# Kernel optimization log

Hardware: AMD Instinct MI355X
Metric: run time of the kernel (lower is better)

Reference implementation:

```python
import jax, jax.numpy as jnp
import numpy as np

B_, L_, DM = 8, 1024, 256
DS, DC, EX = 16, 4, 2
DI = EX * DM            # d_inner = 512
DTR = max(1, DM // 16)  # dt_rank = 16


def setup_inputs() -> dict:
    key = jax.random.key(0)
    ks = iter(jax.random.split(key, 40))
    def n(shape, s=0.02):
        return jax.random.normal(next(ks), shape, jnp.float32) * s
    inp = {"x": jax.random.normal(next(ks), (B_, L_, DM), jnp.float32)}
    inp["norm_g"] = jnp.ones((DM,), jnp.float32)
    inp["norm_b"] = jnp.zeros((DM,), jnp.float32)
    for m in ("f", "b"):
        inp[f"inW_{m}"] = n((DM, 2 * DI))
        inp[f"convW_{m}"] = n((DI, DC))
        inp[f"convB_{m}"] = jnp.zeros((DI,), jnp.float32)
        inp[f"xW_{m}"] = n((DI, DTR + 2 * DS))
        inp[f"dtW_{m}"] = n((DTR, DI))
        inp[f"dtB_{m}"] = jnp.zeros((DI,), jnp.float32)
        # ALog init: log of [1..dState] repeated over dInner rows
        inp[f"ALog_{m}"] = jnp.log(jnp.tile(jnp.arange(1, DS + 1, dtype=jnp.float32), (DI, 1)))
        inp[f"Dp_{m}"] = jnp.ones((DI,), jnp.float32)
        inp[f"outW_{m}"] = n((DI, DM))
    inp["fusW"] = n((2 * DM, DM))
    inp["fusB"] = jnp.zeros((DM,), jnp.float32)
    return inp


def _dw_conv(x, w, b):
    # causal depthwise conv1d: x [B,L,DI], w [DI,DC] -> [B,L,DI]
    xc = jnp.transpose(x, (0, 2, 1))  # B,DI,L
    out = jax.lax.conv_general_dilated(
        xc, w[:, None, :], window_strides=(1,), padding=[(DC - 1, 0)],
        dimension_numbers=("NCH", "OIH", "NCH"), feature_group_count=DI)
    return jnp.transpose(out + b[:, None], (0, 2, 1))


def _ssm(x, xW, dtW, dtB, ALog, Dp):
    # x: [B,L,DI]
    A = -jnp.exp(ALog)                                   # [DI,DS]
    xdbl = x @ xW                                        # [B,L,DTR+2*DS]
    dlt, Bp, Cp = jnp.split(xdbl, [DTR, DTR + DS], axis=-1)
    delta = jax.nn.softplus(dlt @ dtW + dtB)             # [B,L,DI]
    dA = jnp.exp(delta[..., None] * A)                   # [B,L,DI,DS]
    dBx = (delta * x)[..., None] * Bp[:, :, None, :]     # [B,L,DI,DS]

    def step(h, t):
        a, bb, c = t
        h = a * h + bb                                   # [B,DI,DS]
        y = jnp.einsum('bdn,bn->bd', h, c)
        return h, y

    h0 = jnp.zeros((x.shape[0], DI, DS), x.dtype)
    _, ys = jax.lax.scan(step, h0, (jnp.moveaxis(dA, 1, 0),
                                    jnp.moveaxis(dBx, 1, 0),
                                    jnp.moveaxis(Cp, 1, 0)))
    return jnp.moveaxis(ys, 0, 1) + Dp * x               # [B,L,DI]


def _mamba(x, inW, convW, convB, xW, dtW, dtB, ALog, Dp, outW):
    xr = x @ inW                                         # [B,L,2*DI]
    xs, res = jnp.split(xr, 2, axis=-1)
    xs = jax.nn.silu(_dw_conv(xs, convW, convB))
    y = _ssm(xs, xW, dtW, dtB, ALog, Dp)
    return (y * jax.nn.silu(res)) @ outW                 # [B,L,DM]


def reference(x, norm_g, norm_b,
              inW_f, convW_f, convB_f, xW_f, dtW_f, dtB_f, ALog_f, Dp_f, outW_f,
              inW_b, convW_b, convB_b, xW_b, dtW_b, dtB_b, ALog_b, Dp_b, outW_b,
              fusW, fusB):
    # LayerNorm
    mu = x.mean(-1, keepdims=True)
    var = ((x - mu) ** 2).mean(-1, keepdims=True)
    xn = (x - mu) * jax.lax.rsqrt(var + 1e-5) * norm_g + norm_b
    # forward-direction Mamba
    xf = _mamba(xn, inW_f, convW_f, convB_f, xW_f, dtW_f, dtB_f, ALog_f, Dp_f, outW_f)
    # backward-direction Mamba (flip along time)
    xb = _mamba(jnp.flip(xn, 1), inW_b, convW_b, convB_b, xW_b, dtW_b, dtB_b, ALog_b, Dp_b, outW_b)
    xb = jnp.flip(xb, 1)
    fused = jnp.concatenate([xf, xb], axis=-1) @ fusW + fusB
    return x + fused  # dropout is identity in eval
```

## Files before the change

### kernel.cpp

```cpp
#include <hip/hip_runtime.h>
#include <cmath>

typedef __bf16 bf16x8 __attribute__((ext_vector_type(8)));
typedef __bf16 bf16x4 __attribute__((ext_vector_type(4)));
typedef float  f32x4  __attribute__((ext_vector_type(4)));
typedef float  f32x2  __attribute__((ext_vector_type(2)));

#define B_  8
#define L_  1024
#define DM  256
#define DI  512
#define DS  16
#define DTR 16
#define M_  (B_*L_)
#define NC  32
#define CT  32

__device__ inline float softplus_f(float z){
  return (z > 20.f) ? z : __logf(1.f + __expf(z));
}
__device__ inline float silu_f(float z){
  return z / (1.f + __expf(-z));
}

__device__ inline int flag_from_x(const void* x){
  const unsigned short* u = (const unsigned short*)x;
  int lane = threadIdx.x & 63;
  unsigned short v = u[2*lane];
  int e = (v >> 7) & 0xFF;
  unsigned long long m = __ballot(e >= 160 || e < 96);
  return __popcll(m) > 16;
}

struct PrepJob { const void* src; void* dst; int rows; int cols; int f32out; };
struct PrepArgs { PrepJob j[26]; int nj; };
struct TJob { const void* src; __bf16* dst; int R; int C; };
struct TArgs { TJob j[3]; int ntiles[3]; int nj; int ntot; };

__global__ __launch_bounds__(256) void wprep_k(TArgs ta, PrepArgs a, const void* xsrc){
  const int f = flag_from_x(xsrc);
  const int tid = threadIdx.x;
  if ((int)blockIdx.x < ta.ntot){
    __shared__ float tile[64][65];
    int bid = blockIdx.x;
    int jj = 0;
    while (jj < ta.nj-1 && bid >= ta.ntiles[jj]) { bid -= ta.ntiles[jj]; jj++; }
    const TJob J = ta.j[jj];
    const int tpr = J.C >> 6;
    const int tr = bid / tpr, tc = bid - tr*tpr;
    const int r0 = tr*64, c0 = tc*64;
    #pragma unroll
    for (int i=0;i<16;i++){
      int idx = i*256 + tid;
      int r = idx >> 6, c = idx & 63;
      long off = (long)(r0+r)*J.C + c0 + c;
      tile[r][c] = f ? ((const float*)J.src)[off] : (float)((const __bf16*)J.src)[off];
    }
    __syncthreads();
    #pragma unroll
    for (int i=0;i<16;i++){
      int idx = i*256 + tid;
      int c = idx >> 6, r = idx & 63;
      J.dst[(long)(c0+c)*J.R + r0 + r] = (__bf16)tile[r][c];
    }
  } else {
    int e = (blockIdx.x - ta.ntot)*256 + tid;
    #pragma unroll 1
    for (int jj=0; jj<a.nj; jj++){
      int sz = a.j[jj].rows * a.j[jj].cols;
      if (e < sz){
        int cols = a.j[jj].cols;
        int r = e / cols, c = e - r*cols;
        float v = f ? ((const float*)a.j[jj].src)[e] : (float)((const __bf16*)a.j[jj].src)[e];
        if (a.j[jj].f32out) ((float*)a.j[jj].dst)[c*a.j[jj].rows + r] = v;
        else ((__bf16*)a.j[jj].dst)[(long)c*a.j[jj].rows + r] = (__bf16)v;
        return;
      }
      e -= sz;
    }
  }
}

__global__ __launch_bounds__(256) void lnw_k(
    const void* x, const __bf16* g, const __bf16* bb, __bf16* xn,
    const __bf16* fusWt, const __bf16* outWr0, const __bf16* outWr1,
    __bf16* BtC0, __bf16* BtC1)
{
  const int bx = blockIdx.x;
  const int tid = threadIdx.x;
  const int lane = tid & 63;
  const int wid = tid >> 6;

  if (bx < M_/4){
    const int f = flag_from_x(x);
    long row = (long)bx*4 + wid;
    long base = row*DM + lane*4;
    float v0,v1,v2,v3;
    if (f){ f32x4 xv = *(const f32x4*)((const float*)x + base);
            v0=xv[0]; v1=xv[1]; v2=xv[2]; v3=xv[3]; }
    else  { bf16x4 xv = *(const bf16x4*)((const __bf16*)x + base);
            v0=(float)xv[0]; v1=(float)xv[1]; v2=(float)xv[2]; v3=(float)xv[3]; }
    float s = v0+v1+v2+v3;
    float q = v0*v0+v1*v1+v2*v2+v3*v3;
    #pragma unroll
    for (int off=32; off>0; off>>=1){ s += __shfl_xor(s,off); q += __shfl_xor(q,off); }
    float mu = s*(1.f/DM), var = q*(1.f/DM)-mu*mu;
    float rs = rsqrtf(var+1e-5f);
    bf16x4 gv = *(const bf16x4*)(g + lane*4);
    bf16x4 bv = *(const bf16x4*)(bb + lane*4);
    bf16x4 o;
    o[0]=(__bf16)((v0-mu)*rs*(float)gv[0]+(float)bv[0]);
    o[1]=(__bf16)((v1-mu)*rs*(float)gv[1]+(float)bv[1]);
    o[2]=(__bf16)((v2-mu)*rs*(float)gv[2]+(float)bv[2]);
    o[3]=(__bf16)((v3-mu)*rs*(float)gv[3]+(float)bv[3]);
    *(bf16x4*)(xn + base) = o;
  } else {
    int b2 = bx - M_/4;
    int wz  = b2 >> 5;
    int rem = b2 & 31;
    int gx = rem & 3, gy = rem >> 2;
    const __bf16* A  = fusWt + wz*DM;
    const __bf16* Bt = wz ? outWr1 : outWr0;
    __bf16* C = wz ? BtC1 : BtC0;
    const int mBase = (gx*4 + wid)*16;
    const int nBase = gy*64;
    const int lm = lane & 15;
    const int kq = (lane >> 4)*8;
    long aoff = (long)(mBase+lm)*(2*DM) + kq;
    long boff[4];
    #pragma unroll
    for (int j=0;j<4;j++) boff[j] = (long)(nBase+j*16+lm)*DM + kq;
    f32x4 acc[4] = {};
    #pragma unroll
    for (int k0=0;k0<DM;k0+=32){
      bf16x8 af = *(const bf16x8*)(A + aoff + k0);
      bf16x8 bfr[4];
      #pragma unroll
      for (int j=0;j<4;j++) bfr[j] = *(const bf16x8*)(Bt + boff[j] + k0);
      #pragma unroll
      for (int j=0;j<4;j++)
        acc[j] = __builtin_amdgcn_mfma_f32_16x16x32_bf16(af, bfr[j], acc[j], 0,0,0);
    }
    #pragma unroll
    for (int rr=0;rr<4;rr++){
      int r = mBase + (lane>>4)*4 + rr;
      #pragma unroll
      for (int j=0;j<4;j++){
        int c = nBase + j*16 + lm;
        C[(long)r*DI + c] = (__bf16)acc[j][rr];
      }
    }
  }
}

template<int BM,int BN,int KK>
__global__ __launch_bounds__(256) void gemm_in_k(
    const __bf16* A, const __bf16* B0, const __bf16* B1,
    __bf16* xz0, __bf16* xz1, __bf16* res0, __bf16* res1,
    int lda, int ldb)
{
  constexpr int TM = BM/2, TN = BN/2;
  constexpr int WMT = TM/16, WNT = TN/16;
  constexpr int LA = BM/64, LB = BN/64;

  const int dir = blockIdx.z;
  const __bf16* Bt = dir ? B1 : B0;
  __bf16* xz  = dir ? xz1 : xz0;
  __bf16* res = dir ? res1 : res0;
  const int tid  = threadIdx.x;
  const int lane = tid & 63;
  const int wid  = tid >> 6;
  const int wm = wid & 1;
  const int wn = wid >> 1;
  const int mBase = blockIdx.x * BM;
  const int nBase = blockIdx.y * BN;
  const int lm = lane & 15;
  const int kq = (lane >> 4) * 8;

  __shared__ __bf16 As[BM*32];
  __shared__ __bf16 Bs[BN*32];

  const __bf16* aS[LA];
  const __bf16* bS[LB];
  {
    int colk = (tid & 3) * 8;
    #pragma unroll
    for (int ld=0; ld<LA; ld++){
      int r = mBase + ld*64 + (tid >> 2);
      if (dir==1){ int b = r >> 10, t = r & (L_-1); r = (b<<10) + (L_-1-t); }
      aS[ld] = A + (long)r*lda + colk;
    }
    #pragma unroll
    for (int ld=0; ld<LB; ld++){
      int r = nBase + ld*64 + (tid >> 2);
      bS[ld] = Bt + (long)r*ldb + colk;
    }
  }

  f32x4 acc[WMT][WNT] = {};
  for (int k0=0; k0<KK; k0+=32){
    #pragma unroll
    for (int ld=0; ld<LA; ld++)
      __builtin_amdgcn_global_load_lds(
        (const __attribute__((address_space(1))) void*)(aS[ld] + k0),
        (__attribute__((address_space(3))) void*)(&As[ld*2048 + tid*8]), 16, 0, 0);
    #pragma unroll
    for (int ld=0; ld<LB; ld++)
      __builtin_amdgcn_global_load_lds(
        (const __attribute__((address_space(1))) void*)(bS[ld] + k0),
        (__attribute__((address_space(3))) void*)(&Bs[ld*2048 + tid*8]), 16, 0, 0);
    __syncthreads();
    bf16x8 af[WMT], bfr[WNT];
    #pragma unroll
    for (int i=0;i<WMT;i++) af[i]  = *(const bf16x8*)&As[(wm*TM + i*16 + lm)*32 + kq];
    #pragma unroll
    for (int j=0;j<WNT;j++) bfr[j] = *(const bf16x8*)&Bs[(wn*TN + j*16 + lm)*32 + kq];
    #pragma unroll
    for (int i=0;i<WMT;i++)
      #pragma unroll
      for (int j=0;j<WNT;j++)
        acc[i][j] = __builtin_amdgcn_mfma_f32_16x16x32_bf16(af[i], bfr[j], acc[i][j], 0,0,0);
    __syncthreads();
  }

  #pragma unroll
  for (int i=0;i<WMT;i++){
    #pragma unroll
    for (int rr=0;rr<4;rr++){
      int r = mBase + wm*TM + i*16 + (lane>>4)*4 + rr;
      #pragma unroll
      for (int j=0;j<WNT;j++){
        int c = nBase + wn*TN + j*16 + lm;
        float v = acc[i][j][rr];
        if (c < DI) xz[(long)r*DI + c] = (__bf16)v;
        else        res[(long)r*DI + (c-DI)] = (__bf16)v;
      }
    }
  }
}

template<int BM,int BN,int KK>
__global__ __launch_bounds__(256) void gemm_fin_k(
    const __bf16* Af, const __bf16* Ab,
    const __bf16* Bt0, const __bf16* Bt1,
    void* Cout, const __bf16* bias, const void* resid)
{
  constexpr int TM = BM/2, TN = BN/2;
  constexpr int WMT = TM/16, WNT = TN/16;
  constexpr int LA = BM/64, LB = BN/64;

  const int of = flag_from_x(resid);
  const int tid  = threadIdx.x;
  const int lane = tid & 63;
  const int wid  = tid >> 6;
  const int wm = wid & 1;
  const int wn = wid >> 1;
  const int mBase = blockIdx.x * BM;
  const int nBase = blockIdx.y * BN;
  const int lm = lane & 15;
  const int kq = (lane >> 4) * 8;

  __shared__ __bf16 As[BM*32];
  __shared__ __bf16 Bs[BN*32];

  f32x4 acc[WMT][WNT] = {};
  #pragma unroll 1
  for (int dd=0; dd<2; dd++){
    const __bf16* A  = dd ? Ab  : Af;
    const __bf16* Bt = dd ? Bt1 : Bt0;
    const __bf16* aS[LA];
    const __bf16* bS[LB];
    {
      int colk = (tid & 3) * 8;
      #pragma unroll
      for (int ld=0; ld<LA; ld++){
        int r = mBase + ld*64 + (tid >> 2);
        if (dd==1){ int b = r >> 10, t = r & (L_-1); r = (b<<10) + (L_-1-t); }
        aS[ld] = A + (long)r*DI + colk;
      }
      #pragma unroll
      for (int ld=0; ld<LB; ld++){
        int r = nBase + ld*64 + (tid >> 2);
        bS[ld] = Bt + (long)r*DI + colk;
      }
    }
    for (int k0=0; k0<KK; k0+=32){
      #pragma unroll
      for (int ld=0; ld<LA; ld++)
        __builtin_amdgcn_global_load_lds(
          (const __attribute__((address_space(1))) void*)(aS[ld] + k0),
          (__attribute__((address_space(3))) void*)(&As[ld*2048 + tid*8]), 16, 0, 0);
      #pragma unroll
      for (int ld=0; ld<LB; ld++)
        __builtin_amdgcn_global_load_lds(
          (const __attribute__((address_space(1))) void*)(bS[ld] + k0),
          (__attribute__((address_space(3))) void*)(&Bs[ld*2048 + tid*8]), 16, 0, 0);
      __syncthreads();
      bf16x8 af[WMT], bfr[WNT];
      #pragma unroll
      for (int i=0;i<WMT;i++) af[i]  = *(const bf16x8*)&As[(wm*TM + i*16 + lm)*32 + kq];
      #pragma unroll
      for (int j=0;j<WNT;j++) bfr[j] = *(const bf16x8*)&Bs[(wn*TN + j*16 + lm)*32 + kq];
      #pragma unroll
      for (int i=0;i<WMT;i++)
        #pragma unroll
        for (int j=0;j<WNT;j++)
          acc[i][j] = __builtin_amdgcn_mfma_f32_16x16x32_bf16(af[i], bfr[j], acc[i][j], 0,0,0);
      __syncthreads();
    }
  }

  #pragma unroll
  for (int i=0;i<WMT;i++){
    #pragma unroll
    for (int rr=0;rr<4;rr++){
      int r = mBase + wm*TM + i*16 + (lane>>4)*4 + rr;
      #pragma unroll
      for (int j=0;j<WNT;j++){
        int c = nBase + wn*TN + j*16 + lm;
        float v = acc[i][j][rr];
        float rsd = of ? ((const float*)resid)[(long)r*DM + c]
                       : (float)((const __bf16*)resid)[(long)r*DM + c];
        v += (float)bias[c] + rsd;
        if (of) ((float*)Cout)[(long)r*DM + c] = v;
        else    ((__bf16*)Cout)[(long)r*DM + c] = (__bf16)v;
      }
    }
  }
}

__global__ __launch_bounds__(512) void scanA_k(
    const __bf16* xz0, const __bf16* xz1,
    const float* cw0, const float* cw1,
    const __bf16* cb0, const __bf16* cb1,
    const __bf16* xW0, const __bf16* xW1,
    const float* dw0, const float* dw1,
    const __bf16* dtB0, const __bf16* dtB1,
    const float* ALf0, const float* ALf1,
    __bf16* xg0, __bf16* xg1,
    float* sg0, float* sg1,
    float* hend, float* sumd)
{
  const int dir = blockIdx.z;
  const __bf16* xz  = dir ? xz1 : xz0;
  const float*  cw  = dir ? cw1 : cw0;
  const __bf16* cb  = dir ? cb1 : cb0;
  const __bf16* xWt = dir ? xW1 : xW0;
  const float*  dw  = dir ? dw1 : dw0;
  const __bf16* dtB = dir ? dtB1 : dtB0;
  const float*  ALf = dir ? ALf1 : ALf0;
  __bf16*       xg  = dir ? xg1 : xg0;
  float*        sg  = dir ? sg1 : sg0;

  const int b   = blockIdx.y;
  const int c   = blockIdx.x;
  const int tid = threadIdx.x;
  const int lane = tid & 63;
  const int wid  = tid >> 6;
  const int d   = tid;
  const int db  = dir*8 + b;
  const long row0 = (long)b*L_ + (long)c*CT;

  __shared__ __bf16 xs_s[CT*DI];
  __shared__ float  sX[CT][48];

  {
    const float q0 = cw[0*DI+d], q1 = cw[1*DI+d], q2 = cw[2*DI+d], q3 = cw[3*DI+d];
    const float cbv = (float)cb[d];
    int gt0 = c*CT;
    float xm3 = (gt0-3 >= 0) ? (float)xz[(row0-3)*DI + d] : 0.f;
    float xm2 = (gt0-2 >= 0) ? (float)xz[(row0-2)*DI + d] : 0.f;
    float xm1 = (gt0-1 >= 0) ? (float)xz[(row0-1)*DI + d] : 0.f;
    #pragma unroll 8
    for (int t=0;t<CT;t++){
      float xt = (float)xz[(row0+t)*DI + d];
      float av = cbv;
      av += xm3*q0; av += xm2*q1; av += xm1*q2; av += xt*q3;
      __bf16 sv = (__bf16)silu_f(av);
      *(__bf16*)((char*)xs_s + t*1024 + ((2*d) ^ ((t&7)<<4))) = sv;
      xg[(row0+t)*DI + d] = sv;
      xm3 = xm2; xm2 = xm1; xm1 = xt;
    }
  }
  __syncthreads();

  if (wid < 6){
    const int mb = (wid & 1) * 16;
    const int nb = (wid >> 1) * 16;
    const int lm = lane & 15;
    const int kq = (lane >> 4) * 8;
    const int row = mb + lm;
    const char* abase = (const char*)xs_s + row*1024;
    const int rsw = (row&7)<<4;
    const __bf16* Bt = xWt + (long)(nb + lm)*DI + kq;
    f32x4 acc = {};
    #pragma unroll
    for (int k0=0;k0<DI;k0+=32){
      bf16x8 af  = *(const bf16x8*)(abase + (((kq + k0)*2) ^ rsw));
      bf16x8 bfr = *(const bf16x8*)(Bt + k0);
      acc = __builtin_amdgcn_mfma_f32_16x16x32_bf16(af, bfr, acc, 0,0,0);
    }
    #pragma unroll
    for (int rr=0;rr<4;rr++){
      int r = mb + (lane>>4)*4 + rr;
      sX[r][nb + lm] = acc[rr];
      sg[(row0 + r)*48 + nb + lm] = acc[rr];
    }
  }

  f32x2 dw2[8];
  { const f32x4* p = (const f32x4*)(dw + d*DTR);
    #pragma unroll
    for (int q=0;q<4;q++){ f32x4 v=p[q];
      dw2[q*2]   = f32x2{v[0],v[1]};
      dw2[q*2+1] = f32x2{v[2],v[3]}; } }
  float A[16];
  { const f32x4* p = (const f32x4*)(ALf + d*DS);
    #pragma unroll
    for (int q=0;q<4;q++){ f32x4 v=p[q];
      A[q*4]=-__expf(v[0]); A[q*4+1]=-__expf(v[1]); A[q*4+2]=-__expf(v[2]); A[q*4+3]=-__expf(v[3]); } }
  bool pow_ok = true;
  #pragma unroll
  for (int n=0;n<16;n++) pow_ok = pow_ok && (fabsf(A[n] + (float)(n+1)) < 0.003f*(n+1));
  const float dtbv = (float)dtB[d];

  f32x2 h2[8];
  #pragma unroll
  for (int i=0;i<8;i++) h2[i] = f32x2{0.f,0.f};
  float sdelta = 0.f;
  __syncthreads();

  if (pow_ok){
    #pragma unroll 2
    for (int t=0;t<CT;t++){
      f32x2 z2 = f32x2{dtbv, 0.f};
      #pragma unroll
      for (int i=0;i<8;i++){
        f32x2 qv = *(const f32x2*)&sX[t][i*2];
        z2 += qv*dw2[i];
      }
      float delta = softplus_f(z2[0]+z2[1]);
      sdelta += delta;
      float xv = (float)*(const __bf16*)((const char*)xs_s + t*1024 + ((2*d) ^ ((t&7)<<4)));
      float dx = delta*xv;
      f32x2 dx2 = f32x2{dx, dx};
      float e1 = __expf(-delta), e2v = e1*e1;
      f32x2 e22 = f32x2{e2v, e2v};
      f32x2 pw = f32x2{e1, e2v};
      #pragma unroll
      for (int i=0;i<8;i++){
        f32x2 Bv = *(const f32x2*)&sX[t][16+i*2];
        h2[i] = pw*h2[i] + dx2*Bv;
        pw = pw*e22;
      }
    }
  } else {
    #pragma unroll 2
    for (int t=0;t<CT;t++){
      f32x2 z2 = f32x2{dtbv, 0.f};
      #pragma unroll
      for (int i=0;i<8;i++){
        f32x2 qv = *(const f32x2*)&sX[t][i*2];
        z2 += qv*dw2[i];
      }
      float delta = softplus_f(z2[0]+z2[1]);
      sdelta += delta;
      float xv = (float)*(const __bf16*)((const char*)xs_s + t*1024 + ((2*d) ^ ((t&7)<<4)));
      float dx = delta*xv;
      #pragma unroll
      for (int i=0;i<8;i++){
        f32x2 Bv = *(const f32x2*)&sX[t][16+i*2];
        f32x2 pw = f32x2{__expf(delta*A[i*2]), __expf(delta*A[i*2+1])};
        h2[i] = pw*h2[i] + f32x2{dx,dx}*Bv;
      }
    }
  }

  long hb = (((long)db*NC + c)*DI + d)*16;
  f32x4* hp = (f32x4*)(hend + hb);
  #pragma unroll
  for (int q=0;q<4;q++){
    f32x4 v; v[0]=h2[q*2][0]; v[1]=h2[q*2][1]; v[2]=h2[q*2+1][0]; v[3]=h2[q*2+1][1];
    hp[q]=v;
  }
  sumd[((long)db*NC + c)*DI + d] = sdelta;
}

__global__ __launch_bounds__(256) void scanB_k(
    const float* ALf0, const float* ALf1,
    const float* hend, const float* sumd, float* Hbuf)
{
  int gid = blockIdx.x*256 + threadIdx.x;
  int n  = gid & 15;
  int d  = (gid>>4) & 511;
  int db = gid >> 13;
  const float* ALf = (db>=8) ? ALf1 : ALf0;
  float A_dn = -__expf(ALf[d*DS + n]);
  const long base0 = (((long)db*NC)*DI + d)*16 + n;
  const long cstr  = (long)DI*16;
  const long sbase = (long)db*NC*DI + d;
  float H = 0.f;
  #pragma unroll 1
  for (int g=0; g<NC/16; g++){
    float he[16], Sv[16];
    #pragma unroll
    for (int k=0;k<16;k++){
      he[k] = hend[base0 + (long)(g*16+k)*cstr];
      Sv[k] = sumd[sbase + (long)(g*16+k)*DI];
    }
    #pragma unroll
    for (int k=0;k<16;k++){
      Hbuf[base0 + (long)(g*16+k)*cstr] = H;
      H = he[k] + __expf(A_dn*Sv[k])*H;
    }
  }
}

__global__ __launch_bounds__(256, 4) void scanC_k(
    const __bf16* __restrict__ xg0, const __bf16* __restrict__ xg1,
    const float* __restrict__ sg0, const float* __restrict__ sg1,
    __bf16* __restrict__ res0, __bf16* __restrict__ res1,
    const float* __restrict__ dw0, const float* __restrict__ dw1,
    const __bf16* __restrict__ dtB0, const __bf16* __restrict__ dtB1,
    const float* __restrict__ ALf0, const float* __restrict__ ALf1,
    const __bf16* __restrict__ Dp0, const __bf16* __restrict__ Dp1,
    const float* __restrict__ Hbuf)
{
  const int zc  = blockIdx.z;
  const int dir = zc >> 1;
  const int dg  = zc & 1;
  const __bf16* xg  = dir ? xg1 : xg0;
  const float*  sg  = dir ? sg1 : sg0;
  __bf16*       res = dir ? res1 : res0;
  const float*  dw  = dir ? dw1 : dw0;
  const __bf16* dtB = dir ? dtB1 : dtB0;
  const float*  ALf = dir ? ALf1 : ALf0;
  const __bf16* Dp  = dir ? Dp1 : Dp0;

  const int b   = blockIdx.y;
  const int c   = blockIdx.x;
  const int dl  = threadIdx.x;
  const int d   = dg*256 + dl;
  const int db  = dir*8 + b;
  const long row0 = (long)b*L_ + (long)c*CT;

  __shared__ __bf16 xs_l[CT*256];
  __shared__ float  sX[CT][48];

  {
    const __bf16* src = xg + row0*DI + dg*256;
    #pragma unroll
    for (int i=0;i<4;i++){
      int r = i*8 + (dl>>5);
      int cs = (dl&31)*8;
      __builtin_amdgcn_global_load_lds(
        (const __attribute__((address_space(1))) void*)(src + (long)r*DI + cs),
        (__attribute__((address_space(3))) void*)(&xs_l[i*2048 + dl*8]), 16, 0, 0);
    }
  }
  for (int v=dl; v<CT*12; v+=256)
    ((f32x4*)sX)[v] = ((const f32x4*)(sg + row0*48))[v];

  f32x2 dw2[8];
  { const f32x4* p = (const f32x4*)(dw + d*DTR);
    #pragma unroll
    for (int q=0;q<4;q++){ f32x4 v=p[q];
      dw2[q*2]   = f32x2{v[0],v[1]};
      dw2[q*2+1] = f32x2{v[2],v[3]}; } }
  float A[16];
  { const f32x4* p = (const f32x4*)(ALf + d*DS);
    #pragma unroll
    for (int q=0;q<4;q++){ f32x4 v=p[q];
      A[q*4]=-__expf(v[0]); A[q*4+1]=-__expf(v[1]); A[q*4+2]=-__expf(v[2]); A[q*4+3]=-__expf(v[3]); } }
  bool pow_ok = true;
  #pragma unroll
  for (int n=0;n<16;n++) pow_ok = pow_ok && (fabsf(A[n] + (float)(n+1)) < 0.003f*(n+1));
  const float dtbv = (float)dtB[d];
  const float Dpv  = (float)Dp[d];

  f32x2 h2[8];
  { long hb = (((long)db*NC + c)*DI + d)*16;
    const f32x4* p = (const f32x4*)(Hbuf + hb);
    #pragma unroll
    for (int q=0;q<4;q++){ f32x4 v = p[q];
      h2[q*2]   = f32x2{v[0],v[1]};
      h2[q*2+1] = f32x2{v[2],v[3]}; } }
  __syncthreads();

  if (pow_ok){
    #pragma unroll 2
    for (int t=0;t<CT;t++){
      long row = row0 + t;
      f32x2 z2 = f32x2{dtbv, 0.f};
      #pragma unroll
      for (int i=0;i<8;i++){
        f32x2 qv = *(const f32x2*)&sX[t][i*2];
        z2 += qv*dw2[i];
      }
      float delta = softplus_f(z2[0]+z2[1]);
      float xv = (float)xs_l[t*256 + dl];
      float dx = delta*xv;
      f32x2 dx2 = f32x2{dx, dx};
      float e1 = __expf(-delta), e2v = e1*e1;
      f32x2 e22 = f32x2{e2v, e2v};
      f32x2 pw = f32x2{e1, e2v};
      f32x2 p2 = f32x2{0.f, 0.f};
      #pragma unroll
      for (int i=0;i<8;i++){
        f32x2 Bv = *(const f32x2*)&sX[t][16+i*2];
        f32x2 Cv = *(const f32x2*)&sX[t][32+i*2];
        h2[i] = pw*h2[i] + dx2*Bv;
        p2 += h2[i]*Cv;
        pw = pw*e22;
      }
      float yv = p2[0] + p2[1] + Dpv*xv;
      float rv = (float)res[row*DI + d];
      res[row*DI + d] = (__bf16)(yv * silu_f(rv));
    }
  } else {
    #pragma unroll 2
    for (int t=0;t<CT;t++){
      long row = row0 + t;
      f32x2 z2 = f32x2{dtbv, 0.f};
      #pragma unroll
      for (int i=0;i<8;i++){
        f32x2 qv = *(const f32x2*)&sX[t][i*2];
        z2 += qv*dw2[i];
      }
      float delta = softplus_f(z2[0]+z2[1]);
      float xv = (float)xs_l[t*256 + dl];
      float dx = delta*xv;
      f32x2 p2 = f32x2{0.f, 0.f};
      #pragma unroll
      for (int i=0;i<8;i++){
        f32x2 Bv = *(const f32x2*)&sX[t][16+i*2];
        f32x2 Cv = *(const f32x2*)&sX[t][32+i*2];
        f32x2 pw = f32x2{__expf(delta*A[i*2]), __expf(delta*A[i*2+1])};
        h2[i] = pw*h2[i] + f32x2{dx,dx}*Bv;
        p2 += h2[i]*Cv;
      }
      float yv = p2[0] + p2[1] + Dpv*xv;
      float rv = (float)res[row*DI + d];
      res[row*DI + d] = (__bf16)(yv * silu_f(rv));
    }
  }
}

extern "C" void kernel_launch(void* const* d_in, const int* in_sizes, int n_in,
                              void* d_out, int out_size, void* d_ws, size_t ws_size,
                              hipStream_t stream)
{
  const size_t MB = 1u<<20;
  if (ws_size < 160*MB) return;

  char* w = (char*)d_ws;
  __bf16* xz[2]   = {(__bf16*)(w + 0),      (__bf16*)(w + 8*MB)};
  __bf16* res[2]  = {(__bf16*)(w + 16*MB),  (__bf16*)(w + 24*MB)};
  __bf16* xs_g[2] = {(__bf16*)(w + 32*MB),  (__bf16*)(w + 40*MB)};
  __bf16* xn      = (__bf16*)(w + 48*MB);

  char* wp = w + 52*MB;
  auto carve = [&](size_t bytes)->void*{
    void* p = wp;
    wp += (bytes + 255) & ~(size_t)255;
    return p;
  };
  __bf16 *inWt[2], *xWt[2], *outWr[2], *BtC[2];
  float *dtWt[2], *convWt[2];
  for (int m=0;m<2;m++){
    inWt[m]   = (__bf16*)carve((size_t)(2*DI)*DM*2);
    xWt[m]    = (__bf16*)carve((size_t)48*DI*2);
    outWr[m]  = (__bf16*)carve((size_t)DI*DM*2);
    BtC[m]    = (__bf16*)carve((size_t)DM*DI*2);
    dtWt[m]   = (float*)carve((size_t)DI*DTR*4);
    convWt[m] = (float*)carve((size_t)4*DI*4);
  }
  __bf16* fusWt = (__bf16*)carve((size_t)DM*(2*DM)*2);
  float* ALf[2] = {(float*)carve((size_t)DI*DS*4), (float*)carve((size_t)DI*DS*4)};

  char* cp = w + 57*MB;
  auto carve2 = [&](size_t elems)->__bf16*{
    __bf16* p = (__bf16*)cp;
    cp += (elems*2 + 255) & ~(size_t)255;
    return p;
  };
  __bf16* ngc = carve2(DM);
  __bf16* nbc = carve2(DM);
  __bf16 *convBc[2], *dtBc[2], *Dpc[2];
  for (int m=0;m<2;m++){
    convBc[m] = carve2(DI);
    dtBc[m]   = carve2(DI);
    Dpc[m]    = carve2(DI);
  }
  __bf16* fusBc = carve2(DM);

  float* sXg[2] = {(float*)(w + 58*MB), (float*)(w + 60*MB)};
  float* hend = (float*)(w + 90*MB);
  float* Hbuf = (float*)(w + 110*MB);
  float* sumd = (float*)(w + 130*MB);

  PrepArgs pa;
  int ji = 0;
  size_t tot = 0;
  auto addj = [&](const void* s, void* dst, int rows, int cols, int f32o){
    pa.j[ji++] = {s, dst, rows, cols, f32o};
    tot += (size_t)rows*cols;
  };
  for (int m=0;m<2;m++){
    int base = 3 + m*9;
    addj(d_in[base+3], xWt[m],   DI,  48,   0);
    addj(d_in[base+8], outWr[m], 1,   DI*DM,0);
    addj(d_in[base+4], dtWt[m],  DTR, DI,   1);
    addj(d_in[base+1], convWt[m],DI,  4,    1);
    addj(d_in[base+2], convBc[m],1, DI, 0);
    addj(d_in[base+5], dtBc[m],  1, DI, 0);
    addj(d_in[base+6], (void*)ALf[m], 1, DI*DS, 1);
    addj(d_in[base+7], Dpc[m],   1, DI, 0);
  }
  addj(d_in[1],  ngc, 1, DM, 0);
  addj(d_in[2],  nbc, 1, DM, 0);
  addj(d_in[22], fusBc, 1, DM, 0);
  pa.nj = ji;

  TArgs ta;
  ta.j[0] = { d_in[3],  inWt[0], DM,   2*DI }; ta.ntiles[0] = (DM/64)*((2*DI)/64);
  ta.j[1] = { d_in[12], inWt[1], DM,   2*DI }; ta.ntiles[1] = (DM/64)*((2*DI)/64);
  ta.j[2] = { d_in[21], fusWt,   2*DM, DM   }; ta.ntiles[2] = ((2*DM)/64)*(DM/64);
  ta.nj = 3;
  ta.ntot = ta.ntiles[0]+ta.ntiles[1]+ta.ntiles[2];
  int prepBlocks = (int)((tot+255)/256);
  wprep_k<<<ta.ntot + prepBlocks, 256, 0, stream>>>(ta, pa, d_in[0]);

  lnw_k<<<M_/4 + 64, 256, 0, stream>>>(
      d_in[0], ngc, nbc, xn, fusWt, outWr[0], outWr[1], BtC[0], BtC[1]);

  gemm_in_k<128,128,256><<<dim3(M_/128, (2*DI)/128, 2), 256, 0, stream>>>(
      xn, inWt[0], inWt[1], xz[0], xz[1], res[0], res[1], DM, DM);

  scanA_k<<<dim3(NC, B_, 2), 512, 0, stream>>>(
      xz[0], xz[1], convWt[0], convWt[1], convBc[0], convBc[1],
      xWt[0], xWt[1], dtWt[0], dtWt[1],
      dtBc[0], dtBc[1], ALf[0], ALf[1],
      xs_g[0], xs_g[1], sXg[0], sXg[1],
      hend, sumd);
  scanB_k<<<131072/256, 256, 0, stream>>>(ALf[0], ALf[1], hend, sumd, Hbuf);
  scanC_k<<<dim3(NC, B_, 4), 256, 0, stream>>>(
      xs_g[0], xs_g[1], sXg[0], sXg[1], res[0], res[1],
      dtWt[0], dtWt[1], dtBc[0], dtBc[1], ALf[0], ALf[1], Dpc[0], Dpc[1], Hbuf);

  gemm_fin_k<64,64,DI><<<dim3(M_/64, DM/64, 1), 256, 0, stream>>>(
      res[0], res[1], BtC[0], BtC[1], d_out, fusBc, d_in[0]);
}
```

Measured before the change: 234.5 us.

## Merge weight prep and LayerNorm/outW-fusW product into one kernel launch

Folds the LayerNorm and outW·fusW precompute kernel into the weight-prep kernel, so one launch replaces two. The precompute now reads fusW and outW directly from the raw inputs (transposing fusW through shared memory and converting outW on the fly) instead of going through separate prep copies, and LayerNorm reads gamma/beta directly. This removes one kernel launch and several small copy jobs. In exchange the merged kernel uses a larger static shared-memory buffer for every block, which can lower occupancy for the simple elementwise blocks.

Measured after the change: 250.7 us. 6.9% more time.

```diff
diff --git a/kernel.cpp b/kernel.cpp
--- a/kernel.cpp
+++ b/kernel.cpp
@@ -33,21 +33,32 @@
 }
 
 struct PrepJob { const void* src; void* dst; int rows; int cols; int f32out; };
-struct PrepArgs { PrepJob j[26]; int nj; };
+struct PrepArgs { PrepJob j[20]; int nj; };
 struct TJob { const void* src; __bf16* dst; int R; int C; };
-struct TArgs { TJob j[3]; int ntiles[3]; int nj; int ntot; };
-
-__global__ __launch_bounds__(256) void wprep_k(TArgs ta, PrepArgs a, const void* xsrc){
-  const int f = flag_from_x(xsrc);
+struct TArgs { TJob j[2]; int ntiles[2]; int ntot; };
+
+__global__ __launch_bounds__(256) void wprep_k(
+    TArgs ta, PrepArgs a, int prepBlocks,
+    const void* x, const void* gsrc, const void* bsrc, __bf16* xn,
+    const void* fusW, const void* outW0, const void* outW1,
+    __bf16* BtC0, __bf16* BtC1)
+{
+  const int f = flag_from_x(x);
   const int tid = threadIdx.x;
-  if ((int)blockIdx.x < ta.ntot){
-    __shared__ float tile[64][65];
-    int bid = blockIdx.x;
+  const int bid = blockIdx.x;
+  const int lane = tid & 63;
+  const int wid  = tid >> 6;
+
+  __shared__ __align__(16) char smem[64*264*2];
+
+  if (bid < ta.ntot){
+    float (*tile)[65] = (float(*)[65])smem;
+    int b2 = bid;
     int jj = 0;
-    while (jj < ta.nj-1 && bid >= ta.ntiles[jj]) { bid -= ta.ntiles[jj]; jj++; }
+    if (b2 >= ta.ntiles[0]){ b2 -= ta.ntiles[0]; jj = 1; }
     const TJob J = ta.j[jj];
     const int tpr = J.C >> 6;
-    const int tr = bid / tpr, tc = bid - tr*tpr;
+    const int tr = b2 / tpr, tc = b2 - tr*tpr;
     const int r0 = tr*64, c0 = tc*64;
     #pragma unroll
     for (int i=0;i<16;i++){
@@ -63,8 +74,8 @@
       int c = idx >> 6, r = idx & 63;
       J.dst[(long)(c0+c)*J.R + r0 + r] = (__bf16)tile[r][c];
     }
-  } else {
-    int e = (blockIdx.x - ta.ntot)*256 + tid;
+  } else if (bid < ta.ntot + prepBlocks){
+    int e = (bid - ta.ntot)*256 + tid;
     #pragma unroll 1
     for (int jj=0; jj<a.nj; jj++){
       int sz = a.j[jj].rows * a.j[jj].cols;
@@ -78,22 +89,9 @@
       }
       e -= sz;
     }
-  }
-}
-
-__global__ __launch_bounds__(256) void lnw_k(
-    const void* x, const __bf16* g, const __bf16* bb, __bf16* xn,
-    const __bf16* fusWt, const __bf16* outWr0, const __bf16* outWr1,
-    __bf16* BtC0, __bf16* BtC1)
-{
-  const int bx = blockIdx.x;
-  const int tid = threadIdx.x;
-  const int lane = tid & 63;
-  const int wid = tid >> 6;
-
-  if (bx < M_/4){
-    const int f = flag_from_x(x);
-    long row = (long)bx*4 + wid;
+  } else if (bid < ta.ntot + prepBlocks + M_/4){
+    int lnb = bid - (ta.ntot + prepBlocks);
+    long row = (long)lnb*4 + wid;
     long base = row*DM + lane*4;
     float v0,v1,v2,v3;
     if (f){ f32x4 xv = *(const f32x4*)((const float*)x + base);
@@ -106,44 +104,69 @@
     for (int off=32; off>0; off>>=1){ s += __shfl_xor(s,off); q += __shfl_xor(q,off); }
     float mu = s*(1.f/DM), var = q*(1.f/DM)-mu*mu;
     float rs = rsqrtf(var+1e-5f);
-    bf16x4 gv = *(const bf16x4*)(g + lane*4);
-    bf16x4 bv = *(const bf16x4*)(bb + lane*4);
+    float g0,g1,g2,g3,b0,b1,b2,b3;
+    if (f){
+      f32x4 gv = *(const f32x4*)((const float*)gsrc + lane*4);
+      f32x4 bv = *(const f32x4*)((const float*)bsrc + lane*4);
+      g0=gv[0];g1=gv[1];g2=gv[2];g3=gv[3];
+      b0=bv[0];b1=bv[1];b2=bv[2];b3=bv[3];
+    } else {
+      bf16x4 gv = *(const bf16x4*)((const __bf16*)gsrc + lane*4);
+      bf16x4 bv = *(const bf16x4*)((const __bf16*)bsrc + lane*4);
+      g0=(float)gv[0];g1=(float)gv[1];g2=(float)gv[2];g3=(float)gv[3];
+      b0=(float)bv[0];b1=(float)bv[1];b2=(float)bv[2];b3=(float)bv[3];
+    }
     bf16x4 o;
-    o[0]=(__bf16)((v0-mu)*rs*(float)gv[0]+(float)bv[0]);
-    o[1]=(__bf16)((v1-mu)*rs*(float)gv[1]+(float)bv[1]);
-    o[2]=(__bf16)((v2-mu)*rs*(float)gv[2]+(float)bv[2]);
-    o[3]=(__bf16)((v3-mu)*rs*(float)gv[3]+(float)bv[3]);
+    o[0]=(__bf16)((v0-mu)*rs*g0+b0);
+    o[1]=(__bf16)((v1-mu)*rs*g1+b1);
+    o[2]=(__bf16)((v2-mu)*rs*g2+b2);
+    o[3]=(__bf16)((v3-mu)*rs*g3+b3);
     *(bf16x4*)(xn + base) = o;
   } else {
-    int b2 = bx - M_/4;
-    int wz  = b2 >> 5;
-    int rem = b2 & 31;
+    int w2 = bid - (ta.ntot + prepBlocks + M_/4);
+    int wz  = w2 >> 5;
+    int rem = w2 & 31;
     int gx = rem & 3, gy = rem >> 2;
-    const __bf16* A  = fusWt + wz*DM;
-    const __bf16* Bt = wz ? outWr1 : outWr0;
+    const void* outW = wz ? outW1 : outW0;
     __bf16* C = wz ? BtC1 : BtC0;
-    const int mBase = (gx*4 + wid)*16;
-    const int nBase = gy*64;
+    __bf16 (*At)[264] = (__bf16(*)[264])smem;
+    #pragma unroll
+    for (int i=0;i<64;i++){
+      int idx = i*256 + tid;
+      int k = idx >> 6, cc = idx & 63;
+      long off = (long)(wz*DM + k)*DM + gx*64 + cc;
+      float v = f ? ((const float*)fusW)[off] : (float)((const __bf16*)fusW)[off];
+      At[cc][k] = (__bf16)v;
+    }
+    __syncthreads();
     const int lm = lane & 15;
     const int kq = (lane >> 4)*8;
-    long aoff = (long)(mBase+lm)*(2*DM) + kq;
-    long boff[4];
-    #pragma unroll
-    for (int j=0;j<4;j++) boff[j] = (long)(nBase+j*16+lm)*DM + kq;
+    const int nBase = gy*64;
     f32x4 acc[4] = {};
     #pragma unroll
     for (int k0=0;k0<DM;k0+=32){
-      bf16x8 af = *(const bf16x8*)(A + aoff + k0);
+      bf16x8 af = *(const bf16x8*)&At[wid*16 + lm][kq + k0];
       bf16x8 bfr[4];
       #pragma unroll
-      for (int j=0;j<4;j++) bfr[j] = *(const bf16x8*)(Bt + boff[j] + k0);
+      for (int j=0;j<4;j++){
+        long o = (long)(nBase + j*16 + lm)*DM + kq + k0;
+        if (f){
+          const float* op = (const float*)outW + o;
+          bf16x8 t;
+          #pragma unroll
+          for (int qi=0;qi<8;qi++) t[qi] = (__bf16)op[qi];
+          bfr[j] = t;
+        } else {
+          bfr[j] = *(const bf16x8*)((const __bf16*)outW + o);
+        }
+      }
       #pragma unroll
       for (int j=0;j<4;j++)
         acc[j] = __builtin_amdgcn_mfma_f32_16x16x32_bf16(af, bfr[j], acc[j], 0,0,0);
     }
     #pragma unroll
     for (int rr=0;rr<4;rr++){
-      int r = mBase + (lane>>4)*4 + rr;
+      int r = gx*64 + wid*16 + (lane>>4)*4 + rr;
       #pragma unroll
       for (int j=0;j<4;j++){
         int c = nBase + j*16 + lm;
@@ -665,17 +688,15 @@
     wp += (bytes + 255) & ~(size_t)255;
     return p;
   };
-  __bf16 *inWt[2], *xWt[2], *outWr[2], *BtC[2];
+  __bf16 *inWt[2], *xWt[2], *BtC[2];
   float *dtWt[2], *convWt[2];
   for (int m=0;m<2;m++){
     inWt[m]   = (__bf16*)carve((size_t)(2*DI)*DM*2);
     xWt[m]    = (__bf16*)carve((size_t)48*DI*2);
-    outWr[m]  = (__bf16*)carve((size_t)DI*DM*2);
     BtC[m]    = (__bf16*)carve((size_t)DM*DI*2);
     dtWt[m]   = (float*)carve((size_t)DI*DTR*4);
     convWt[m] = (float*)carve((size_t)4*DI*4);
   }
-  __bf16* fusWt = (__bf16*)carve((size_t)DM*(2*DM)*2);
   float* ALf[2] = {(float*)carve((size_t)DI*DS*4), (float*)carve((size_t)DI*DS*4)};
 
   char* cp = w + 57*MB;
@@ -684,8 +705,6 @@
     cp += (elems*2 + 255) & ~(size_t)255;
     return p;
   };
-  __bf16* ngc = carve2(DM);
-  __bf16* nbc = carve2(DM);
   __bf16 *convBc[2], *dtBc[2], *Dpc[2];
   for (int m=0;m<2;m++){
     convBc[m] = carve2(DI);
@@ -709,7 +728,6 @@
   for (int m=0;m<2;m++){
     int base = 3 + m*9;
     addj(d_in[base+3], xWt[m],   DI,  48,   0);
-    addj(d_in[base+8], outWr[m], 1,   DI*DM,0);
     addj(d_in[base+4], dtWt[m],  DTR, DI,   1);
     addj(d_in[base+1], convWt[m],DI,  4,    1);
     addj(d_in[base+2], convBc[m],1, DI, 0);
@@ -717,22 +735,19 @@
     addj(d_in[base+6], (void*)ALf[m], 1, DI*DS, 1);
     addj(d_in[base+7], Dpc[m],   1, DI, 0);
   }
-  addj(d_in[1],  ngc, 1, DM, 0);
-  addj(d_in[2],  nbc, 1, DM, 0);
   addj(d_in[22], fusBc, 1, DM, 0);
   pa.nj = ji;
 
   TArgs ta;
-  ta.j[0] = { d_in[3],  inWt[0], DM,   2*DI }; ta.ntiles[0] = (DM/64)*((2*DI)/64);
-  ta.j[1] = { d_in[12], inWt[1], DM,   2*DI }; ta.ntiles[1] = (DM/64)*((2*DI)/64);
-  ta.j[2] = { d_in[21], fusWt,   2*DM, DM   }; ta.ntiles[2] = ((2*DM)/64)*(DM/64);
-  ta.nj = 3;
-  ta.ntot = ta.ntiles[0]+ta.ntiles[1]+ta.ntiles[2];
+  ta.j[0] = { d_in[3],  inWt[0], DM, 2*DI }; ta.ntiles[0] = (DM/64)*((2*DI)/64);
+  ta.j[1] = { d_in[12], inWt[1], DM, 2*DI }; ta.ntiles[1] = (DM/64)*((2*DI)/64);
+  ta.ntot = ta.ntiles[0] + ta.ntiles[1];
   int prepBlocks = (int)((tot+255)/256);
-  wprep_k<<<ta.ntot + prepBlocks, 256, 0, stream>>>(ta, pa, d_in[0]);
-
-  lnw_k<<<M_/4 + 64, 256, 0, stream>>>(
-      d_in[0], ngc, nbc, xn, fusWt, outWr[0], outWr[1], BtC[0], BtC[1]);
+  int gridTot = ta.ntot + prepBlocks + M_/4 + 64;
+  wprep_k<<<gridTot, 256, 0, stream>>>(
+      ta, pa, prepBlocks,
+      d_in[0], d_in[1], d_in[2], xn,
+      d_in[21], d_in[11], d_in[20], BtC[0], BtC[1]);
 
   gemm_in_k<128,128,256><<<dim3(M_/128, (2*DI)/128, 2), 256, 0, stream>>>(
       xn, inWt[0], inWt[1], xz[0], xz[1], res[0], res[1], DM, DM);
```
